# Performance work log

Measured on AMD Instinct MI355X. Metric: run time of the kernel, lower is better.

The kernel has to match this reference:

```python
import jax, jax.numpy as jnp
import numpy as np

B = 1024      # batch
V = 5023      # FLAME vertices
NF = 9976     # FLAME faces
NJ = 5        # joints: global, neck, jaw, eyeL, eyeR
NL = 51       # static landmarks
PARENTS = (-1, 0, 1, 1, 1)


def setup_inputs() -> dict:
    key = jax.random.key(0)
    ks = jax.random.split(key, 16)
    inp = {}
    # trainable flame parameters (small pose magnitudes for realism)
    inp['shape_params'] = jax.random.normal(ks[0], (B, 300), jnp.float32)
    inp['expression_params'] = jax.random.normal(ks[1], (B, 100), jnp.float32)
    inp['global_rot'] = 0.1 * jax.random.normal(ks[2], (B, 3), jnp.float32)
    inp['neck_pose'] = 0.1 * jax.random.normal(ks[3], (B, 3), jnp.float32)
    inp['jaw_pose'] = 0.1 * jax.random.normal(ks[4], (B, 3), jnp.float32)
    inp['eye_pose'] = 0.1 * jax.random.normal(ks[5], (B, 6), jnp.float32)
    inp['transl'] = jax.random.normal(ks[6], (B, 3), jnp.float32)
    # flame buffers
    inp['v_template'] = jax.random.normal(ks[7], (V, 3), jnp.float32)
    inp['shapedirs'] = 0.01 * jax.random.normal(ks[8], (V, 3, 400), jnp.float32)
    inp['posedirs'] = 0.01 * jax.random.normal(ks[9], (36, V * 3), jnp.float32)
    Jreg = jax.random.uniform(ks[10], (NJ, V), jnp.float32)
    inp['J_regressor'] = Jreg / jnp.sum(Jreg, axis=1, keepdims=True)
    W = jax.random.uniform(ks[11], (V, NJ), jnp.float32)
    inp['lbs_weights'] = W / jnp.sum(W, axis=1, keepdims=True)
    bc = jax.random.uniform(ks[12], (NL, 3), jnp.float32)
    inp['lmk_bary_coords'] = bc / jnp.sum(bc, axis=1, keepdims=True)
    inp['parents'] = jnp.array(PARENTS, dtype=jnp.int32)
    inp['faces'] = jax.random.randint(ks[13], (NF, 3), 0, V, jnp.int32)
    inp['lmk_faces_idx'] = jax.random.randint(ks[14], (NL,), 0, NF, jnp.int64)
    return inp


def batch_rodrigues(rvecs):
    # rvecs: [N,3] axis-angle -> [N,3,3] rotation matrices
    angle = jnp.sqrt(jnp.sum(jnp.square(rvecs + 1e-8), axis=1, keepdims=True))  # [N,1]
    axis = rvecs / angle
    s = jnp.sin(angle)[:, :, None]
    c = jnp.cos(angle)[:, :, None]
    rx, ry, rz = axis[:, 0], axis[:, 1], axis[:, 2]
    zeros = jnp.zeros_like(rx)
    K = jnp.stack([zeros, -rz, ry, rz, zeros, -rx, -ry, rx, zeros], axis=1).reshape(-1, 3, 3)
    I = jnp.eye(3, dtype=rvecs.dtype)
    return I + s * K + (1.0 - c) * (K @ K)


def _lbs(betas, full_pose, v_template, shapedirs, posedirs, J_regressor, lbs_weights):
    b = betas.shape[0]
    # shape+expression blendshapes
    v_shaped = v_template[None] + jnp.einsum('bl,vkl->bvk', betas, shapedirs)  # [B,V,3]
    joints = jnp.einsum('jv,bvk->bjk', J_regressor, v_shaped)                 # [B,J,3]
    rot_mats = batch_rodrigues(full_pose.reshape(-1, 3)).reshape(b, NJ, 3, 3)
    # pose blendshapes (exclude root)
    ident = jnp.eye(3, dtype=betas.dtype)
    pose_feature = (rot_mats[:, 1:] - ident).reshape(b, 9 * (NJ - 1))         # [B,36]
    v_posed = v_shaped + (pose_feature @ posedirs).reshape(b, V, 3)
    # rigid kinematic chain
    rel_joints = jnp.concatenate(
        [joints[:, :1], joints[:, 1:] - joints[:, jnp.array(PARENTS[1:])]], axis=1)
    bottom = jnp.broadcast_to(jnp.array([0., 0., 0., 1.], betas.dtype), (b, NJ, 1, 4))
    tf = jnp.concatenate(
        [jnp.concatenate([rot_mats, rel_joints[..., None]], axis=3), bottom], axis=2)  # [B,J,4,4]
    chain = [tf[:, 0]]
    for i in range(1, NJ):
        chain.append(chain[PARENTS[i]] @ tf[:, i])
    transforms = jnp.stack(chain, axis=1)                                    # [B,J,4,4]
    # remove rest-pose joint location from translation column
    jh = jnp.einsum('bjmn,bjn->bjm', transforms[:, :, :3, :3], joints)       # [B,J,3]
    A = transforms.at[:, :, :3, 3].add(-jh)
    # skinning
    T = jnp.einsum('vj,bjmn->bvmn', lbs_weights, A)                          # [B,V,4,4]
    v_h = jnp.concatenate([v_posed, jnp.ones((b, V, 1), betas.dtype)], axis=2)
    verts = jnp.einsum('bvmn,bvn->bvm', T, v_h)[..., :3]                     # [B,V,3]
    return verts, transforms[:, :, :3, 3]


def reference(shape_params, expression_params, global_rot, neck_pose, jaw_pose,
              eye_pose, transl, v_template, shapedirs, posedirs, J_regressor,
              lbs_weights, lmk_bary_coords, parents, faces, lmk_faces_idx):
    betas = jnp.concatenate([shape_params, expression_params], axis=1)       # [B,400]
    full_pose = jnp.concatenate([global_rot, neck_pose, jaw_pose, eye_pose], axis=1)  # [B,15]
    vertices, _ = _lbs(betas, full_pose, v_template, shapedirs, posedirs,
                       J_regressor, lbs_weights)
    # barycentric landmark interpolation
    lmk_faces = faces[lmk_faces_idx]                                         # [L,3]
    lmk_verts = vertices[:, lmk_faces]                                       # [B,L,3,3]
    landmarks_3d = jnp.einsum('blfk,lf->blk', lmk_verts, lmk_bary_coords)    # [B,L,3]
    landmarks_3d = landmarks_3d + transl[:, None]
    vertices = vertices + transl[:, None]
    # default-weights flame regularizer (fixed_shape=None, ref_vertices=None)
    flame_reg = (100.0 * jnp.sum(neck_pose ** 2)
                 + 0.001 * jnp.sum(jaw_pose ** 2)
                 + 0.001 * jnp.sum(shape_params ** 2)
                 + 0.001 * jnp.sum(expression_params ** 2))
    return vertices, landmarks_3d, flame_reg
```

## Files before the change

kernel.cpp:

```cpp
#include <hip/hip_runtime.h>
#include <hip/hip_bf16.h>

#define BATCH 1024
#define NV 5023
#define NJOINT 5
#define NLMK 51
#define N3 (NV*3)
#define NPADB 15072
#define KBETA 400
#define KTOT 448
#define NSTEP 14
#define RB_B (NPADB/16)
#define RB_A 64
#define FRAG 512

#define BM 64
#define BN 48

#define PK_BETA_CH (NPADB*50)
#define PK_BETA_BLKS 2944
#define PK_POSE_CH (RB_B*96)
#define PK_POSE_BLKS 354
#define NVC2 360
#define VCH 14
#define PK_JS_BLKS (3*NVC2)

#define GBM 64
#define GBN 192
#define GNP 79
#define GGRID 1280
#define CH_S 52

typedef __attribute__((ext_vector_type(8))) short short8;
typedef __attribute__((ext_vector_type(4))) float floatx4;
typedef __attribute__((ext_vector_type(4))) float float4v;

#define GLDS16(gp, lp) \
    __builtin_amdgcn_global_load_lds( \
        (const __attribute__((address_space(1))) void*)(gp), \
        (__attribute__((address_space(3))) void*)(lp), 16, 0, 0)

#define WS_JS      0
#define WS_BASEJ   24064
#define WS_REG     24512
#define WS_FLAGS   24520
#define WS_AMAT    24576
#define WS_ACT     270336
#define WS_WB      1187840
#define WS_FULL    14692352

__device__ __forceinline__ float ldf(const void* p, long i, int f32) {
    if (f32) return ((const float*)p)[i];
    return __bfloat162float(((const __hip_bfloat16*)p)[i]);
}
__device__ __forceinline__ short8 ld8bf(const void* p, long i, int f32) {
    if (f32) {
        float4v a = *(const float4v*)((const float*)p + i);
        float4v b = *(const float4v*)((const float*)p + i + 4);
        short8 r;
#pragma unroll
        for (int j = 0; j < 4; ++j) {
            __hip_bfloat16 h = __float2bfloat16(a[j]);
            r[j] = *reinterpret_cast<short*>(&h);
        }
#pragma unroll
        for (int j = 0; j < 4; ++j) {
            __hip_bfloat16 h = __float2bfloat16(b[j]);
            r[4 + j] = *reinterpret_cast<short*>(&h);
        }
        return r;
    }
    return *(const short8*)((const __hip_bfloat16*)p + i);
}
__device__ __forceinline__ void stf(void* p, long i, float v, int f32) {
    if (f32) ((float*)p)[i] = v;
    else ((__hip_bfloat16*)p)[i] = __float2bfloat16(v);
}

__device__ __forceinline__ long act2_off(int b, int k) {
    return (((long)(k >> 5) * RB_A + (b >> 4)) * 64 + ((k >> 3) & 3) * 16 + (b & 15)) * 8 + (k & 7);
}

__device__ __forceinline__ int probe_f32(const void* shape_p) {
    int lane = threadIdx.x & 63;
    unsigned short h = ((const unsigned short*)shape_p)[2 * lane];
    union { unsigned short u; __hip_bfloat16 b; } cv; cv.u = h;
    float v = fabsf(__bfloat162float(cv.b));
    if (v != v) v = 3.4e38f;
#pragma unroll
    for (int off = 32; off; off >>= 1) v = fmaxf(v, __shfl_down(v, off));
    v = __shfl(v, 0);
    return v > 1e4f;
}
__device__ __forceinline__ int probe_i64(const void* lmk_idx) {
    int lane = threadIdx.x & 63;
    const int* q = (const int*)lmk_idx;
    int odd_nonzero = (lane < 25) && (q[2*lane + 1] != 0);
    unsigned long long b = __ballot(odd_nonzero);
    return b == 0ull;
}

__global__ void k_init(float* ws0, const void* shape_p, const void* lmk_idx, int* flags) {
    int i = blockIdx.x * 256 + threadIdx.x;
    if (i < 6129) ws0[i] = 0.f;
    if (blockIdx.x == 0 && threadIdx.x < 64) {
        int f = probe_f32(shape_p);
        int i64 = probe_i64(lmk_idx);
        if (threadIdx.x == 0) { flags[0] = f; flags[1] = i64; }
    }
}

__global__ __launch_bounds__(256) void k_prep(const void* __restrict__ shapedirs,
                                              const void* __restrict__ posedirs,
                                              const void* __restrict__ Jreg,
                                              const void* __restrict__ v_template,
                                              const void* __restrict__ shape_p,
                                              float* __restrict__ reg,
                                              __hip_bfloat16* __restrict__ Wb,
                                              float* __restrict__ PART) {
    __shared__ float jl[NJOINT * VCH];
    int f32 = probe_f32(shape_p);
    int blk = blockIdx.x, tid = threadIdx.x;
    if (blk < PK_BETA_BLKS) {
        if (blk == 0 && tid == 0) reg[0] = 0.f;
        int g = blk * 256 + tid;
        if (g >= PK_BETA_CH) return;
        int n = g / 50, kg = g - n * 50;
        short8 o;
#pragma unroll
        for (int e = 0; e < 8; ++e) o[e] = 0;
        if (n < N3) o = ld8bf(shapedirs, (long)n * KBETA + kg * 8, f32);
        long chunk = ((long)(kg >> 2) * RB_B + (n >> 4)) * 64 + (kg & 3) * 16 + (n & 15);
        *(short8*)(Wb + chunk * 8) = o;
    } else if (blk < PK_BETA_BLKS + PK_POSE_BLKS) {
        int g = (blk - PK_BETA_BLKS) * 256 + tid;
        if (g >= PK_POSE_CH) return;
        int R = g / 96, rem = g - R * 96;
        int c = rem >> 4, fr = rem & 15;
        int n = R * 16 + fr;
        int k0 = KBETA + 8 * c;
        short8 o;
#pragma unroll
        for (int e = 0; e < 8; ++e) o[e] = 0;
        if (n < N3) {
#pragma unroll
            for (int e = 0; e < 8; ++e) {
                int kk = k0 + e - KBETA;
                float val = (kk < 36) ? ldf(posedirs, (long)kk * N3 + n, f32) : 0.f;
                __hip_bfloat16 h = __float2bfloat16(val);
                o[e] = *reinterpret_cast<short*>(&h);
            }
        }
        long chunk = ((long)(k0 >> 5) * RB_B + R) * 64 + ((k0 >> 3) & 3) * 16 + fr;
        *(short8*)(Wb + chunk * 8) = o;
    } else {
        int b2 = blk - (PK_BETA_BLKS + PK_POSE_BLKS);
        int k = b2 / NVC2;
        int vc = b2 - k * NVC2;
        int v0 = vc * VCH;
        if (tid < NJOINT * VCH) {
            int j = tid / VCH, i = tid - j * VCH;
            int v = min(v0 + i, NV - 1);
            jl[tid] = ldf(Jreg, (long)j * NV + v, f32);
        }
        __syncthreads();
        int l2 = tid + 256;
        float acc1[NJOINT] = {0,0,0,0,0};
        float acc2[NJOINT] = {0,0,0,0,0};
#pragma unroll
        for (int i = 0; i < VCH; ++i) {
            int v = v0 + i;
            if (v >= NV) break;
            float s1 = ldf(shapedirs, (long)v*1200 + k*400 + tid, f32);
            float s2 = 0.f;
            if (l2 < 400)       s2 = ldf(shapedirs, (long)v*1200 + k*400 + l2, f32);
            else if (l2 == 400) s2 = ldf(v_template, v*3 + k, f32);
#pragma unroll
            for (int j = 0; j < NJOINT; ++j) {
                float jr = jl[j*VCH + i];
                acc1[j] += jr * s1;
                acc2[j] += jr * s2;
            }
        }
        long base = ((long)(k*NVC2 + vc)*5)*401;
#pragma unroll
        for (int j = 0; j < NJOINT; ++j) {
            PART[base + j*401 + tid] = acc1[j];
            if (l2 <= 400) PART[base + j*401 + l2] = acc2[j];
        }
    }
}

__global__ __launch_bounds__(256) void k_js_red(const float* __restrict__ PART,
                                                float* __restrict__ JS,
                                                float* __restrict__ baseJ) {
    int o = blockIdx.x * 256 + threadIdx.x;
    if (o >= 3*5*401) return;
    int k = o / 2005, r = o - k*2005;
    int j = r / 401, l = r - j*401;
    float s = 0.f;
    long base = ((long)(k*NVC2)*5 + j)*401 + l;
    for (int vc = 0; vc < NVC2; ++vc) s += PART[base + (long)vc*2005];
    if (l < 400) JS[j*1200 + k*400 + l] = s;
    else         baseJ[j*3 + k] = s;
}

__global__ void k_js_atomic(const void* __restrict__ Jreg,
                            const void* __restrict__ shapedirs,
                            const void* __restrict__ v_template,
                            const int* __restrict__ flags,
                            float* __restrict__ JS, float* __restrict__ baseJ) {
    int f32 = flags[0];
    int k = blockIdx.x, vc = blockIdx.y, tid = threadIdx.x;
    int v0 = vc * 79, v1 = min(NV, v0 + 79);
    int l2 = tid + 256;
    float acc1[NJOINT] = {0,0,0,0,0};
    float acc2[NJOINT] = {0,0,0,0,0};
    for (int v = v0; v < v1; ++v) {
        float s1 = ldf(shapedirs, (long)v*1200 + k*400 + tid, f32);
        float s2 = 0.f;
        if (l2 < 400)       s2 = ldf(shapedirs, (long)v*1200 + k*400 + l2, f32);
        else if (l2 == 400) s2 = ldf(v_template, v*3 + k, f32);
#pragma unroll
        for (int j = 0; j < NJOINT; ++j) {
            float jr = ldf(Jreg, j*NV + v, f32);
            acc1[j] += jr * s1;
            acc2[j] += jr * s2;
        }
    }
#pragma unroll
    for (int j = 0; j < NJOINT; ++j) {
        atomicAdd(&JS[j*1200 + k*400 + tid], acc1[j]);
        if (l2 < 400)       atomicAdd(&JS[j*1200 + k*400 + l2], acc2[j]);
        else if (l2 == 400) atomicAdd(&baseJ[j*3 + k], acc2[j]);
    }
}

__global__ __launch_bounds__(64) void k_batch(
        const void* __restrict__ shape_p, const void* __restrict__ expr_p,
        const void* __restrict__ grot, const void* __restrict__ neck,
        const void* __restrict__ jaw,  const void* __restrict__ eye,
        const float* __restrict__ JS, const float* __restrict__ baseJ,
        __hip_bfloat16* __restrict__ Act, float* __restrict__ Amat, float* __restrict__ reg) {
    int f32 = probe_f32(shape_p);
    int b = blockIdx.x, tid = threadIdx.x;
    __shared__ float betas[400];
    __shared__ float Rm[NJOINT][9];
    __shared__ float joints[NJOINT][3];
    __shared__ float Gm[NJOINT][12];

    for (int i = tid; i < 400; i += 64) {
        float v = (i < 300) ? ldf(shape_p, b*300 + i, f32)
                            : ldf(expr_p, b*100 + i - 300, f32);
        betas[i] = v;
        Act[act2_off(b, i)] = __float2bfloat16(v);
    }
    if (tid >= 36 && tid < 48) Act[act2_off(b, 400 + tid)] = __float2bfloat16(0.f);
    __syncthreads();

    if (tid < 60) {
        int o = tid % 15, q = tid / 15;
        int j = o / 3, kk = o - 3*j;
        const float* js = &JS[j*1200 + kk*400 + q*100];
        float s = 0.f;
        for (int l = 0; l < 100; ++l) s += js[l] * betas[q*100 + l];
        s += __shfl_down(s, 15);
        s += __shfl_down(s, 30);
        if (q == 0) joints[j][kk] = s + baseJ[o];
    }
    if (tid < NJOINT) {
        int j = tid;
        float r[3];
        for (int c = 0; c < 3; ++c) {
            if (j == 0)      r[c] = ldf(grot, b*3 + c, f32);
            else if (j == 1) r[c] = ldf(neck, b*3 + c, f32);
            else if (j == 2) r[c] = ldf(jaw,  b*3 + c, f32);
            else if (j == 3) r[c] = ldf(eye,  b*6 + c, f32);
            else             r[c] = ldf(eye,  b*6 + 3 + c, f32);
        }
        float a0 = r[0] + 1e-8f, a1 = r[1] + 1e-8f, a2 = r[2] + 1e-8f;
        float angle = sqrtf(a0*a0 + a1*a1 + a2*a2);
        float inv = 1.0f / angle;
        float rx = r[0]*inv, ry = r[1]*inv, rz = r[2]*inv;
        float s = sinf(angle), c = cosf(angle);
        float K[9] = {0.f, -rz, ry,  rz, 0.f, -rx,  -ry, rx, 0.f};
        float K2[9];
        for (int rr = 0; rr < 3; ++rr)
            for (int cc = 0; cc < 3; ++cc) {
                float t = 0.f;
                for (int m = 0; m < 3; ++m) t += K[rr*3+m] * K[m*3+cc];
                K2[rr*3+cc] = t;
            }
        for (int i2 = 0; i2 < 9; ++i2) {
            float id = (i2 == 0 || i2 == 4 || i2 == 8) ? 1.f : 0.f;
            Rm[j][i2] = id + s*K[i2] + (1.f - c)*K2[i2];
        }
    }
    __syncthreads();

    if (tid < 36) {
        int i = tid / 9 + 1, rc = tid - (tid/9)*9;
        float id = (rc == 0 || rc == 4 || rc == 8) ? 1.f : 0.f;
        Act[act2_off(b, 400 + tid)] = __float2bfloat16(Rm[i][rc] - id);
    }
    if (tid == 0) {
        for (int rr = 0; rr < 3; ++rr) {
            for (int cc = 0; cc < 3; ++cc) Gm[0][rr*4+cc] = Rm[0][rr*3+cc];
            Gm[0][rr*4+3] = joints[0][rr];
        }
        const int par[NJOINT] = {-1, 0, 1, 1, 1};
        for (int j = 1; j < NJOINT; ++j) {
            int p = par[j];
            float rel[3];
            for (int c2 = 0; c2 < 3; ++c2) rel[c2] = joints[j][c2] - joints[p][c2];
            for (int rr = 0; rr < 3; ++rr) {
                for (int cc = 0; cc < 3; ++cc) {
                    float t = 0.f;
                    for (int m = 0; m < 3; ++m) t += Gm[p][rr*4+m] * Rm[j][m*3+cc];
                    Gm[j][rr*4+cc] = t;
                }
                float t = Gm[p][rr*4+3];
                for (int m = 0; m < 3; ++m) t += Gm[p][rr*4+m] * rel[m];
                Gm[j][rr*4+3] = t;
            }
        }
    }
    __syncthreads();

    if (tid < 60) {
        int j = tid / 12, e = tid - j*12, rr = e / 4, cc = e - rr*4;
        float val = Gm[j][e];
        if (cc == 3)
            for (int m = 0; m < 3; ++m) val -= Gm[j][rr*4+m] * joints[j][m];
        Amat[b*60 + tid] = val;
    }

    float part = 0.f;
    for (int i = tid; i < 400; i += 64) part += betas[i]*betas[i];
    part *= 0.001f;
    if (tid == 0) {
        float nn = 0.f, jj = 0.f;
        for (int c = 0; c < 3; ++c) {
            float nv = ldf(neck, b*3+c, f32);
            float jv = ldf(jaw,  b*3+c, f32);
            nn += nv*nv; jj += jv*jv;
        }
        part += 100.f*nn + 0.001f*jj;
    }
    for (int off = 32; off; off >>= 1) part += __shfl_down(part, off);
    if (tid == 0) atomicAdd(reg, part);
}

__global__ __launch_bounds__(512, 2) void k_gemm_lbs_big(
        const __hip_bfloat16* __restrict__ Act,
        const __hip_bfloat16* __restrict__ Wb,
        const void* __restrict__ v_template,
        const float* __restrict__ Amat,
        const void* __restrict__ weights,
        const void* __restrict__ transl,
        const void* __restrict__ shape_p,
        void* __restrict__ out) {
    __shared__ __align__(16) __hip_bfloat16 stage[2][16 * FRAG];
    __shared__ float chunk[8][16 * CH_S];
    __shared__ float Al[GBM * 60];
    __shared__ float wl[64 * 5];
    __shared__ float tl[GBM * 3];
    __shared__ float vtl[GBN];

    int f32 = probe_f32(shape_p);
    int tid = threadIdx.x;
    int wave = tid >> 6, lane = tid & 63;
    int fr = lane & 15, quad = lane >> 4;
    int mg = wave >> 2, wn = wave & 3;

    int lin = blockIdx.x;
    int xcd = lin & 7, slot = lin >> 3;
    int P = (slot >> 4) * 8 + xcd;
    int mblk = slot & 15;
    if (P >= GNP) return;
    int m0 = mblk * GBM;
    int v0 = P * 64;

    for (int i = tid; i < GBM*60/4; i += 512)
        ((float4v*)Al)[i] = ((const float4v*)(Amat + (long)m0*60))[i];
    if (tid < 320) {
        int v = v0 + tid / 5;
        wl[tid] = (v < NV) ? ldf(weights, v*5 + tid % 5, f32) : 0.f;
    }
    if (tid < GBM*3)
        tl[tid] = ldf(transl, (long)m0*3 + tid, f32);
    if (tid >= 320) {
        int i = tid - 320;
        vtl[i] = ((long)v0*3 + i < N3) ? ldf(v_template, (long)v0*3 + i, f32) : 0.f;
    }

    int r0 = wave*2, r1 = wave*2 + 1;
    long aoff0 = 0, aoff1 = 0;
    const __hip_bfloat16* base0;
    const __hip_bfloat16* base1;
    int sstr0, sstr1;
    {
        if (r0 < 4) { base0 = Act; sstr0 = RB_A; aoff0 = mblk*4 + r0; }
        else {
            long rb = (long)P*12 + (r0 - 4);
            if (rb > RB_B-1) rb = RB_B-1;
            base0 = Wb; sstr0 = RB_B; aoff0 = rb;
        }
        if (r1 < 4) { base1 = Act; sstr1 = RB_A; aoff1 = mblk*4 + r1; }
        else {
            long rb = (long)P*12 + (r1 - 4);
            if (rb > RB_B-1) rb = RB_B-1;
            base1 = Wb; sstr1 = RB_B; aoff1 = rb;
        }
    }
    __hip_bfloat16* lds0[2] = { &stage[0][r0*FRAG], &stage[1][r0*FRAG] };
    __hip_bfloat16* lds1[2] = { &stage[0][r1*FRAG], &stage[1][r1*FRAG] };

    floatx4 acc[2][3];
#pragma unroll
    for (int q = 0; q < 2; ++q)
#pragma unroll
        for (int t = 0; t < 3; ++t) acc[q][t] = (floatx4){0.f,0.f,0.f,0.f};

    asm volatile("s_waitcnt vmcnt(0)" ::: "memory");
    __builtin_amdgcn_sched_barrier(0);
    GLDS16(base0 + ((long)0*sstr0 + aoff0)*FRAG + lane*8, lds0[0]);
    GLDS16(base1 + ((long)0*sstr1 + aoff1)*FRAG + lane*8, lds1[0]);
    GLDS16(base0 + ((long)1*sstr0 + aoff0)*FRAG + lane*8, lds0[1]);
    GLDS16(base1 + ((long)1*sstr1 + aoff1)*FRAG + lane*8, lds1[1]);

#pragma unroll
    for (int s = 0; s < NSTEP; ++s) {
        const int cb = s & 1;
        if (s == NSTEP-1) { asm volatile("s_waitcnt vmcnt(0)" ::: "memory"); }
        else              { asm volatile("s_waitcnt vmcnt(2)" ::: "memory"); }
        __builtin_amdgcn_sched_barrier(0);
        __builtin_amdgcn_s_barrier();
        __builtin_amdgcn_sched_barrier(0);
        const __hip_bfloat16* sb = stage[cb];
        short8 a0 = *(const short8*)&sb[(mg*2 + 0)*FRAG + lane*8];
        short8 a1 = *(const short8*)&sb[(mg*2 + 1)*FRAG + lane*8];
        short8 b0 = *(const short8*)&sb[(4 + wn*3 + 0)*FRAG + lane*8];
        short8 b1 = *(const short8*)&sb[(4 + wn*3 + 1)*FRAG + lane*8];
        short8 b2 = *(const short8*)&sb[(4 + wn*3 + 2)*FRAG + lane*8];
        acc[0][0] = __builtin_amdgcn_mfma_f32_16x16x32_bf16(a0, b0, acc[0][0], 0, 0, 0);
        acc[0][1] = __builtin_amdgcn_mfma_f32_16x16x32_bf16(a0, b1, acc[0][1], 0, 0, 0);
        acc[0][2] = __builtin_amdgcn_mfma_f32_16x16x32_bf16(a0, b2, acc[0][2], 0, 0, 0);
        acc[1][0] = __builtin_amdgcn_mfma_f32_16x16x32_bf16(a1, b0, acc[1][0], 0, 0, 0);
        acc[1][1] = __builtin_amdgcn_mfma_f32_16x16x32_bf16(a1, b1, acc[1][1], 0, 0, 0);
        acc[1][2] = __builtin_amdgcn_mfma_f32_16x16x32_bf16(a1, b2, acc[1][2], 0, 0, 0);
        __builtin_amdgcn_sched_barrier(0);
        __builtin_amdgcn_s_barrier();
        __builtin_amdgcn_sched_barrier(0);
        if (s + 2 < NSTEP) {
            GLDS16(base0 + ((long)(s+2)*sstr0 + aoff0)*FRAG + lane*8, lds0[cb]);
            GLDS16(base1 + ((long)(s+2)*sstr1 + aoff1)*FRAG + lane*8, lds1[cb]);
        }
    }

    __syncthreads();
    float* ch = chunk[wave];
    int mloc = lane >> 2, vq = lane & 3;
#pragma unroll
    for (int q = 0; q < 2; ++q) {
#pragma unroll
        for (int t = 0; t < 3; ++t)
#pragma unroll
            for (int rr = 0; rr < 4; ++rr)
                ch[(quad*4 + rr)*CH_S + t*16 + fr] = acc[q][t][rr];
        __syncthreads();
        int mb = mg*32 + q*16 + mloc;
        long mglob = m0 + mb;
        const float* A = &Al[mb*60];
        float t0c = tl[mb*3+0], t1c = tl[mb*3+1], t2c = tl[mb*3+2];
        long obase = (mglob*NV + v0)*3;
#pragma unroll
        for (int vi = 0; vi < 4; ++vi) {
            int vloc = wn*16 + vq*4 + vi;
            int v = v0 + vloc;
            if (v < NV) {
                int o = mloc*CH_S + (vq*4 + vi)*3;
                float p0 = ch[o+0] + vtl[vloc*3 + 0];
                float p1 = ch[o+1] + vtl[vloc*3 + 1];
                float p2 = ch[o+2] + vtl[vloc*3 + 2];
                float w0 = wl[vloc*5+0], w1 = wl[vloc*5+1], w2 = wl[vloc*5+2];
                float w3 = wl[vloc*5+3], w4 = wl[vloc*5+4];
#pragma unroll
                for (int c = 0; c < 3; ++c) {
                    float t0 = w0*A[c*4+0] + w1*A[12+c*4+0] + w2*A[24+c*4+0] + w3*A[36+c*4+0] + w4*A[48+c*4+0];
                    float t1 = w0*A[c*4+1] + w1*A[12+c*4+1] + w2*A[24+c*4+1] + w3*A[36+c*4+1] + w4*A[48+c*4+1];
                    float t2 = w0*A[c*4+2] + w1*A[12+c*4+2] + w2*A[24+c*4+2] + w3*A[36+c*4+2] + w4*A[48+c*4+2];
                    float t3 = w0*A[c*4+3] + w1*A[12+c*4+3] + w2*A[24+c*4+3] + w3*A[36+c*4+3] + w4*A[48+c*4+3];
                    float tlc = (c == 0) ? t0c : ((c == 1) ? t1c : t2c);
                    float val = t0*p0 + t1*p1 + t2*p2 + t3 + tlc;
                    stf(out, obase + vloc*3 + c, val, f32);
                }
            }
        }
        __syncthreads();
    }
}

__global__ __launch_bounds__(256) void k_gemm_lbs_small(
        const __hip_bfloat16* __restrict__ Act,
        const void* __restrict__ shapedirs,
        const void* __restrict__ posedirs,
        const void* __restrict__ v_template,
        const float* __restrict__ Amat,
        const void* __restrict__ weights,
        const void* __restrict__ transl,
        const int* __restrict__ flags,
        void* __restrict__ out) {
    __shared__ float tileS[4][16*49 + 4];
    __shared__ float AlS[4][960];
    __shared__ float wl[80];
    __shared__ __align__(16) __hip_bfloat16 Bs2[BN * 64];

    int f32 = flags[0];
    int tid = threadIdx.x;
    int wave = tid >> 6, lane = tid & 63;
    int fr = lane & 15, quad = lane >> 4;
    int m0 = blockIdx.x * 256;
    int n0 = blockIdx.y * BN;
    int v0 = blockIdx.y * 16;

    if (tid < 80) {
        int v = v0 + tid / 5;
        wl[tid] = (v < NV) ? ldf(weights, v*5 + tid % 5, f32) : 0.f;
    }
    for (int i = tid; i < BN * 64; i += 256) {
        int n = i >> 6, kk = i & 63;
        int nc = min(n0 + n, N3 - 1);
        float val = 0.f;
        if (kk < 16)      val = ldf(shapedirs, (long)nc*KBETA + 384 + kk, f32);
        else if (kk < 52) val = ldf(posedirs, (long)(kk-16)*N3 + nc, f32);
        Bs2[n*64 + kk] = __float2bfloat16(val);
    }
    __syncthreads();

    int Ra0 = (m0 >> 4) + wave*4;
    int nr[3];
#pragma unroll
    for (int t = 0; t < 3; ++t) nr[t] = min(n0 + t*16 + fr, N3 - 1);

    floatx4 acc[4][3];
#pragma unroll
    for (int sub = 0; sub < 4; ++sub)
#pragma unroll
        for (int t = 0; t < 3; ++t) acc[sub][t] = (floatx4){0.f,0.f,0.f,0.f};

#pragma unroll
    for (int s = 0; s < 14; ++s) {
        short8 bb[3];
#pragma unroll
        for (int t = 0; t < 3; ++t) {
            if (s < 12) bb[t] = ld8bf(shapedirs, (long)nr[t]*KBETA + s*32 + quad*8, f32);
            else        bb[t] = *(short8*)&Bs2[(t*16 + fr)*64 + (s-12)*32 + quad*8];
        }
#pragma unroll
        for (int sub = 0; sub < 4; ++sub) {
            short8 a = *(const short8*)(Act + (((long)s*RB_A + Ra0 + sub)*64 + lane)*8);
#pragma unroll
            for (int t = 0; t < 3; ++t)
                acc[sub][t] = __builtin_amdgcn_mfma_f32_16x16x32_bf16(a, bb[t], acc[sub][t], 0, 0, 0);
        }
    }

    int vloc = fr, rgrp = quad;
    int v = v0 + vloc;
    float tpl0 = 0.f, tpl1 = 0.f, tpl2 = 0.f;
    if (v < NV) {
        tpl0 = ldf(v_template, v*3 + 0, f32);
        tpl1 = ldf(v_template, v*3 + 1, f32);
        tpl2 = ldf(v_template, v*3 + 2, f32);
    }
    float w0 = wl[vloc*5+0], w1 = wl[vloc*5+1], w2 = wl[vloc*5+2];
    float w3 = wl[vloc*5+3], w4 = wl[vloc*5+4];
    for (int sub = 0; sub < 4; ++sub) {
#pragma unroll
        for (int t = 0; t < 3; ++t)
#pragma unroll
            for (int rr = 0; rr < 4; ++rr)
                tileS[wave][(quad*4 + rr)*49 + t*16 + fr] = acc[sub][t][rr];
        for (int i = lane; i < 960; i += 64)
            AlS[wave][i] = Amat[(long)(m0 + wave*64 + sub*16)*60 + i];
        __syncthreads();
        if (v < NV) {
#pragma unroll
            for (int rr = 0; rr < 4; ++rr) {
                int mloc = rgrp*4 + rr;
                long m = m0 + wave*64 + sub*16 + mloc;
                float p0 = tileS[wave][mloc*49 + vloc*3 + 0] + tpl0;
                float p1 = tileS[wave][mloc*49 + vloc*3 + 1] + tpl1;
                float p2 = tileS[wave][mloc*49 + vloc*3 + 2] + tpl2;
                const float* A = &AlS[wave][mloc*60];
#pragma unroll
                for (int c = 0; c < 3; ++c) {
                    float t0 = w0*A[c*4+0] + w1*A[12+c*4+0] + w2*A[24+c*4+0] + w3*A[36+c*4+0] + w4*A[48+c*4+0];
                    float t1 = w0*A[c*4+1] + w1*A[12+c*4+1] + w2*A[24+c*4+1] + w3*A[36+c*4+1] + w4*A[48+c*4+1];
                    float t2 = w0*A[c*4+2] + w1*A[12+c*4+2] + w2*A[24+c*4+2] + w3*A[36+c*4+2] + w4*A[48+c*4+2];
                    float t3 = w0*A[c*4+3] + w1*A[12+c*4+3] + w2*A[24+c*4+3] + w3*A[36+c*4+3] + w4*A[48+c*4+3];
                    float val = t0*p0 + t1*p1 + t2*p2 + t3 + ldf(transl, m*3 + c, f32);
                    stf(out, (m*NV + v)*3 + c, val, f32);
                }
            }
        }
        __syncthreads();
    }
}

__global__ __launch_bounds__(64) void k_lmk(const void* __restrict__ verts,
                                            const void* __restrict__ bary,
                                            const int* __restrict__ faces,
                                            const void* __restrict__ lmk_idx,
                                            const void* __restrict__ transl,
                                            const float* __restrict__ reg,
                                            const void* __restrict__ shape_p,
                                            void* __restrict__ out) {
    int f32 = probe_f32(shape_p);
    int i64 = probe_i64(lmk_idx);
    int b = blockIdx.x, tid = threadIdx.x;
    if (b == 0 && tid == 63)
        stf(out, (long)BATCH*NV*3 + (long)BATCH*NLMK*3, reg[0], f32);
    if (tid >= NLMK) return;
    int f = i64 ? (int)((const long long*)lmk_idx)[tid]
                : ((const int*)lmk_idx)[tid];
    float acc[3] = {0.f, 0.f, 0.f};
    float bsum = 0.f;
    for (int fi = 0; fi < 3; ++fi) {
        int vi = faces[f*3 + fi];
        float bc = ldf(bary, tid*3 + fi, f32);
        bsum += bc;
#pragma unroll
        for (int c = 0; c < 3; ++c)
            acc[c] += bc * ldf(verts, ((long)b*NV + vi)*3 + c, f32);
    }
#pragma unroll
    for (int c = 0; c < 3; ++c) {
        float val = acc[c] + (1.f - bsum) * ldf(transl, b*3 + c, f32);
        stf(out, (long)BATCH*NV*3 + ((long)b*NLMK + tid)*3 + c, val, f32);
    }
}

extern "C" void kernel_launch(void* const* d_in, const int* in_sizes, int n_in,
                              void* d_out, int out_size, void* d_ws, size_t ws_size,
                              hipStream_t stream) {
    const void* shape_p   = d_in[0];
    const void* expr_p    = d_in[1];
    const void* grot      = d_in[2];
    const void* neck      = d_in[3];
    const void* jaw       = d_in[4];
    const void* eye       = d_in[5];
    const void* transl    = d_in[6];
    const void* v_templ   = d_in[7];
    const void* shapedirs = d_in[8];
    const void* posedirs  = d_in[9];
    const void* Jreg      = d_in[10];
    const void* weights   = d_in[11];
    const void* bary      = d_in[12];
    const int*  faces     = (const int*)d_in[14];
    const void* lmk_idx   = d_in[15];

    char* ws = (char*)d_ws;
    float* JS      = (float*)(ws + WS_JS);
    float* baseJ   = (float*)(ws + WS_BASEJ);
    float* reg     = (float*)(ws + WS_REG);
    int*   flags   = (int*)(ws + WS_FLAGS);
    float* Amat    = (float*)(ws + WS_AMAT);
    __hip_bfloat16* Act = (__hip_bfloat16*)(ws + WS_ACT);
    __hip_bfloat16* Wb  = (__hip_bfloat16*)(ws + WS_WB);
    float* PART    = (float*)d_out;
    bool big = ws_size >= (size_t)WS_FULL;

    if (big) {
        k_prep<<<PK_BETA_BLKS + PK_POSE_BLKS + PK_JS_BLKS, 256, 0, stream>>>(
            shapedirs, posedirs, Jreg, v_templ, shape_p, reg, Wb, PART);
        k_js_red<<<24, 256, 0, stream>>>(PART, JS, baseJ);
    } else {
        k_init<<<24, 256, 0, stream>>>((float*)ws, shape_p, lmk_idx, flags);
        k_js_atomic<<<dim3(3, 64), 256, 0, stream>>>(Jreg, shapedirs, v_templ, flags, JS, baseJ);
    }
    k_batch<<<BATCH, 64, 0, stream>>>(shape_p, expr_p, grot, neck, jaw, eye,
                                      JS, baseJ, Act, Amat, reg);
    if (big) {
        k_gemm_lbs_big<<<GGRID, 512, 0, stream>>>(Act, Wb, v_templ, Amat,
                                                  weights, transl, shape_p, d_out);
    } else {
        dim3 grid(BATCH/256, (N3 + BN - 1)/BN);
        k_gemm_lbs_small<<<grid, 256, 0, stream>>>(Act, shapedirs, posedirs, v_templ,
                                                   Amat, weights, transl, flags, d_out);
    }
    k_lmk<<<BATCH, 64, 0, stream>>>(d_out, bary, faces, lmk_idx, transl, reg, shape_p, d_out);
}
```

Measured before the change: 254.5 us.

## Stage LBS epilogue outputs in LDS for coalesced stores; split JS reduction

The GEMM epilogue now assigns one vertex per lane and writes the skinned results into a reused LDS staging buffer. The whole block then writes contiguous rows of the output tensor, so global stores are coalesced instead of strided per-thread scalar writes. The joint-shape reduction is split six ways along the vertex-chunk axis and combined with atomicAdds, with k_prep zeroing the JS and baseJ targets first. The cost is extra barriers and LDS traffic in the epilogue, plus float atomics that make the JS sums order-nondeterministic.

Result: faster. 214.8 us (-15.6%).

```diff
diff --git a/kernel.cpp b/kernel.cpp
--- a/kernel.cpp
+++ b/kernel.cpp
@@ -30,6 +30,7 @@
 #define GNP 79
 #define GGRID 1280
 #define CH_S 52
+#define CH_PAD 4
 
 typedef __attribute__((ext_vector_type(8))) short short8;
 typedef __attribute__((ext_vector_type(4))) float floatx4;
@@ -116,6 +117,8 @@
                                               const void* __restrict__ v_template,
                                               const void* __restrict__ shape_p,
                                               float* __restrict__ reg,
+                                              float* __restrict__ JS,
+                                              float* __restrict__ baseJ,
                                               __hip_bfloat16* __restrict__ Wb,
                                               float* __restrict__ PART) {
     __shared__ float jl[NJOINT * VCH];
@@ -123,6 +126,11 @@
     int blk = blockIdx.x, tid = threadIdx.x;
     if (blk < PK_BETA_BLKS) {
         if (blk == 0 && tid == 0) reg[0] = 0.f;
+        if (blk < 24) {
+            int zi = blk * 256 + tid;
+            if (zi < 6000) JS[zi] = 0.f;
+            if (zi < 15) baseJ[zi] = 0.f;
+        }
         int g = blk * 256 + tid;
         if (g >= PK_BETA_CH) return;
         int n = g / 50, kg = g - n * 50;
@@ -196,13 +204,14 @@
                                                 float* __restrict__ baseJ) {
     int o = blockIdx.x * 256 + threadIdx.x;
     if (o >= 3*5*401) return;
+    int g = blockIdx.y;
     int k = o / 2005, r = o - k*2005;
     int j = r / 401, l = r - j*401;
     float s = 0.f;
-    long base = ((long)(k*NVC2)*5 + j)*401 + l;
-    for (int vc = 0; vc < NVC2; ++vc) s += PART[base + (long)vc*2005];
-    if (l < 400) JS[j*1200 + k*400 + l] = s;
-    else         baseJ[j*3 + k] = s;
+    long base = ((long)(k*NVC2 + g*60)*5 + j)*401 + l;
+    for (int vc = 0; vc < 60; ++vc) s += PART[base + (long)vc*2005];
+    if (l < 400) atomicAdd(&JS[j*1200 + k*400 + l], s);
+    else         atomicAdd(&baseJ[j*3 + k], s);
 }
 
 __global__ void k_js_atomic(const void* __restrict__ Jreg,
@@ -361,7 +370,7 @@
         const void* __restrict__ shape_p,
         void* __restrict__ out) {
     __shared__ __align__(16) __hip_bfloat16 stage[2][16 * FRAG];
-    __shared__ float chunk[8][16 * CH_S];
+    __shared__ float chunk[8][16 * CH_S + CH_PAD];
     __shared__ float Al[GBM * 60];
     __shared__ float wl[64 * 5];
     __shared__ float tl[GBM * 3];
@@ -459,8 +468,14 @@
     }
 
     __syncthreads();
+    float* vbuf = (float*)stage;
     float* ch = chunk[wave];
-    int mloc = lane >> 2, vq = lane & 3;
+    int mloc_w = lane;
+    float w0 = wl[mloc_w*5+0], w1 = wl[mloc_w*5+1], w2 = wl[mloc_w*5+2];
+    float w3 = wl[mloc_w*5+3], w4 = wl[mloc_w*5+4];
+    float vt0 = vtl[mloc_w*3+0], vt1 = vtl[mloc_w*3+1], vt2 = vtl[mloc_w*3+2];
+    int coff = (mloc_w & 15) * 3;
+    int wnl = mloc_w >> 4;
 #pragma unroll
     for (int q = 0; q < 2; ++q) {
 #pragma unroll
@@ -469,32 +484,37 @@
             for (int rr = 0; rr < 4; ++rr)
                 ch[(quad*4 + rr)*CH_S + t*16 + fr] = acc[q][t][rr];
         __syncthreads();
-        int mb = mg*32 + q*16 + mloc;
-        long mglob = m0 + mb;
-        const float* A = &Al[mb*60];
-        float t0c = tl[mb*3+0], t1c = tl[mb*3+1], t2c = tl[mb*3+2];
-        long obase = (mglob*NV + v0)*3;
-#pragma unroll
-        for (int vi = 0; vi < 4; ++vi) {
-            int vloc = wn*16 + vq*4 + vi;
-            int v = v0 + vloc;
+        int v = v0 + mloc_w;
+#pragma unroll
+        for (int it = 0; it < 4; ++it) {
+            int r32 = it*8 + wave;
+            int mb = ((r32 & 16) << 1) + q*16 + (r32 & 15);
+            const float* A = &Al[mb*60];
+            const float* cc2 = &chunk[((r32 >> 4) << 2) + wnl][(r32 & 15)*CH_S + coff];
             if (v < NV) {
-                int o = mloc*CH_S + (vq*4 + vi)*3;
-                float p0 = ch[o+0] + vtl[vloc*3 + 0];
-                float p1 = ch[o+1] + vtl[vloc*3 + 1];
-                float p2 = ch[o+2] + vtl[vloc*3 + 2];
-                float w0 = wl[vloc*5+0], w1 = wl[vloc*5+1], w2 = wl[vloc*5+2];
-                float w3 = wl[vloc*5+3], w4 = wl[vloc*5+4];
+                float p0 = cc2[0] + vt0;
+                float p1 = cc2[1] + vt1;
+                float p2 = cc2[2] + vt2;
+                float* vb = &vbuf[r32*192 + mloc_w*3];
 #pragma unroll
                 for (int c = 0; c < 3; ++c) {
                     float t0 = w0*A[c*4+0] + w1*A[12+c*4+0] + w2*A[24+c*4+0] + w3*A[36+c*4+0] + w4*A[48+c*4+0];
                     float t1 = w0*A[c*4+1] + w1*A[12+c*4+1] + w2*A[24+c*4+1] + w3*A[36+c*4+1] + w4*A[48+c*4+1];
                     float t2 = w0*A[c*4+2] + w1*A[12+c*4+2] + w2*A[24+c*4+2] + w3*A[36+c*4+2] + w4*A[48+c*4+2];
                     float t3 = w0*A[c*4+3] + w1*A[12+c*4+3] + w2*A[24+c*4+3] + w3*A[36+c*4+3] + w4*A[48+c*4+3];
-                    float tlc = (c == 0) ? t0c : ((c == 1) ? t1c : t2c);
-                    float val = t0*p0 + t1*p1 + t2*p2 + t3 + tlc;
-                    stf(out, obase + vloc*3 + c, val, f32);
+                    vb[c] = t0*p0 + t1*p1 + t2*p2 + t3 + tl[mb*3+c];
                 }
+            }
+        }
+        __syncthreads();
+#pragma unroll
+        for (int it = 0; it < 12; ++it) {
+            int idx = it*512 + tid;
+            int r32 = idx / 192;
+            int col = idx - r32*192;
+            if (v0*3 + col < N3) {
+                int mb = ((r32 & 16) << 1) + q*16 + (r32 & 15);
+                stf(out, ((long)(m0 + mb)*NV + v0)*3 + col, vbuf[idx], f32);
             }
         }
         __syncthreads();
@@ -674,8 +694,8 @@
 
     if (big) {
         k_prep<<<PK_BETA_BLKS + PK_POSE_BLKS + PK_JS_BLKS, 256, 0, stream>>>(
-            shapedirs, posedirs, Jreg, v_templ, shape_p, reg, Wb, PART);
-        k_js_red<<<24, 256, 0, stream>>>(PART, JS, baseJ);
+            shapedirs, posedirs, Jreg, v_templ, shape_p, reg, JS, baseJ, Wb, PART);
+        k_js_red<<<dim3(24, 6), 256, 0, stream>>>(PART, JS, baseJ);
     } else {
         k_init<<<24, 256, 0, stream>>>((float*)ws, shape_p, lmk_idx, flags);
         k_js_atomic<<<dim3(3, 64), 256, 0, stream>>>(Jreg, shapedirs, v_templ, flags, JS, baseJ);
```
